# Kernel optimization log

Hardware: AMD Instinct MI355X
Metric: run time of the kernel (lower is better)

The kernel has to match this reference:

```python
import jax, jax.numpy as jnp
import numpy as np

M, K, N = 8192, 4096, 4096


def setup_inputs() -> dict:
    key = jax.random.key(0)
    k1, k2, k3 = jax.random.split(key, 3)
    x = jax.random.normal(k1, (M, K), dtype=jnp.float32)
    # int8 weight stored post-patch as [in_features, out_features] (cutlass [K, N] layout)
    weight = jax.random.randint(k2, (K, N), -128, 128, dtype=jnp.int32)
    bias = jax.random.normal(k3, (N,), dtype=jnp.float32) * 0.1
    # static per-tensor scales (scalar Parameters of shape [1])
    input_scale = jnp.array([0.02], dtype=jnp.float32)
    weight_scale = jnp.array([0.01], dtype=jnp.float32)
    return {"x": x, "weight": weight, "bias": bias,
            "input_scale": input_scale, "weight_scale": weight_scale}


def reference(x, weight, bias, input_scale, weight_scale):
    # ops.scaled_int8_quant(x, input_scale, symmetric=True):
    # static per-tensor symmetric quantization to int8
    x_q = jnp.clip(jnp.round(x / input_scale), -128, 127).astype(jnp.int8)  # [M, K]
    # scale_a * scale_b, fused bias add, output in x.dtype
    acc = jax.lax.dot_general(
        x_q, weight.astype(jnp.int8),
        dimension_numbers=(((1,), (0,)), ((), ())),
        preferred_element_type=jnp.int32,
    )  # [M, N] int32
    out = acc.astype(x.dtype) * (input_scale * weight_scale) + bias.astype(x.dtype)
    return out
```

## Files before the change

kernel.cpp:

```cpp
#include <hip/hip_runtime.h>
#include <hip/hip_bf16.h>


#define M_DIM 8192
#define K_DIM 4096
#define N_DIM 4096

typedef int i32x4 __attribute__((ext_vector_type(4)));

__device__ __forceinline__ void async_ld16(const void* g, void* l) {
  __builtin_amdgcn_global_load_lds(
      (const __attribute__((address_space(1))) void*)g,
      (__attribute__((address_space(3))) void*)l, 16, 0, 0);
}

__global__ __launch_bounds__(256) void quant_x(const float* __restrict__ x,
                                               const float* __restrict__ sptr,
                                               char* __restrict__ xq) {
  const float s = sptr[0];
  const size_t base = ((size_t)blockIdx.x * 256 + threadIdx.x) * 16;
  const float4* xv = (const float4*)(x + base);
  union { char c[16]; i32x4 v; } u;
#pragma unroll
  for (int q = 0; q < 4; ++q) {
    float4 f = xv[q];
    float a = fminf(127.f, fmaxf(-128.f, rintf(f.x / s)));
    float b = fminf(127.f, fmaxf(-128.f, rintf(f.y / s)));
    float c = fminf(127.f, fmaxf(-128.f, rintf(f.z / s)));
    float d = fminf(127.f, fmaxf(-128.f, rintf(f.w / s)));
    u.c[q * 4 + 0] = (char)(int)a;
    u.c[q * 4 + 1] = (char)(int)b;
    u.c[q * 4 + 2] = (char)(int)c;
    u.c[q * 4 + 3] = (char)(int)d;
  }
  *(i32x4*)(xq + base) = u.v;
}

__global__ __launch_bounds__(256) void wconv(const int* __restrict__ w,
                                             char* __restrict__ bt) {
  __shared__ alignas(16) char tile[64][80];
  const int k0 = blockIdx.x * 64;
  const int n0 = blockIdx.y * 64;
  const int t = threadIdx.x;
  const int kr = t >> 4;
  const int nc = (t & 15) * 4;
#pragma unroll
  for (int it = 0; it < 4; ++it) {
    int k = it * 16 + kr;
    int4 v = *(const int4*)(w + (size_t)(k0 + k) * N_DIM + n0 + nc);
    tile[nc + 0][k] = (char)v.x;
    tile[nc + 1][k] = (char)v.y;
    tile[nc + 2][k] = (char)v.z;
    tile[nc + 3][k] = (char)v.w;
  }
  __syncthreads();
  const int n = t >> 2;
  const int ks = (t & 3) * 16;
  int4 o = *(const int4*)&tile[n][ks];
  *(int4*)(bt + (size_t)(n0 + n) * K_DIM + k0 + ks) = o;
}

__global__ __launch_bounds__(256) void gemm_i8(
    const char* __restrict__ Aq, const char* __restrict__ Bt,
    const float* __restrict__ bias,
    const float* __restrict__ is_ptr, const float* __restrict__ ws_ptr,
    float* __restrict__ out) {
  __shared__ alignas(16) char ldsA[128 * 128];
  __shared__ alignas(16) char ldsB[128 * 128];

  const int nbn = N_DIM / 128;
  const int bid = blockIdx.x;
  const int cpx = gridDim.x >> 3;
  const int swz = (bid & 7) * cpx + (bid >> 3);
  const int bm0 = (swz / nbn) * 128;
  const int bn0 = (swz % nbn) * 128;

  const int t = threadIdx.x;
  const int lane = t & 63;
  const int wave = t >> 6;
  const int wm = wave >> 1;
  const int wn = wave & 1;
  const int lr = lane & 15;
  const int lkb = (lane >> 4) << 4;

  const int sr = t >> 3;
  const int sc = ((t & 7) ^ (sr & 7)) << 4;
  const char* aSrc = Aq + (size_t)(bm0 + sr) * K_DIM + sc;
  const char* bSrc = Bt + (size_t)(bn0 + sr) * K_DIM + sc;
  char* aDst = &ldsA[t * 16];
  char* bDst = &ldsB[t * 16];

  int aOff[4][2], bOff[4][2];
#pragma unroll
  for (int m = 0; m < 4; ++m) {
    int row = wm * 64 + m * 16 + lr;
#pragma unroll
    for (int ks = 0; ks < 2; ++ks) {
      int col = ks * 64 + lkb;
      aOff[m][ks] = row * 128 + (col ^ ((row & 7) << 4));
    }
  }
#pragma unroll
  for (int n = 0; n < 4; ++n) {
    int row = wn * 64 + n * 16 + lr;
#pragma unroll
    for (int ks = 0; ks < 2; ++ks) {
      int col = ks * 64 + lkb;
      bOff[n][ks] = row * 128 + (col ^ ((row & 7) << 4));
    }
  }

  i32x4 acc[4][4];
#pragma unroll
  for (int m = 0; m < 4; ++m)
#pragma unroll
    for (int n = 0; n < 4; ++n) acc[m][n] = (i32x4)(0);

  const int NT = K_DIM / 128;
  for (int kt = 0; kt < NT; ++kt) {
    const size_t ko = (size_t)kt * 128;
#pragma unroll
    for (int it = 0; it < 4; ++it) {
      async_ld16(aSrc + ko + (size_t)it * 32 * K_DIM, aDst + it * 4096);
      async_ld16(bSrc + ko + (size_t)it * 32 * K_DIM, bDst + it * 4096);
    }
    __syncthreads();
#pragma unroll
    for (int ks = 0; ks < 2; ++ks) {
      i32x4 aF[4], bF[4];
#pragma unroll
      for (int m = 0; m < 4; ++m) aF[m] = *(const i32x4*)&ldsA[aOff[m][ks]];
#pragma unroll
      for (int n = 0; n < 4; ++n) bF[n] = *(const i32x4*)&ldsB[bOff[n][ks]];
#pragma unroll
      for (int m = 0; m < 4; ++m)
#pragma unroll
        for (int n = 0; n < 4; ++n)
          acc[m][n] = __builtin_amdgcn_mfma_i32_16x16x64_i8(aF[m], bF[n],
                                                            acc[m][n], 0, 0, 0);
    }
    __syncthreads();
  }

  const float s = is_ptr[0] * ws_ptr[0];
  const int colBase = bn0 + wn * 64 + lr;
  float bv[4];
#pragma unroll
  for (int n = 0; n < 4; ++n) bv[n] = bias[colBase + n * 16];
  const int rowBase = bm0 + wm * 64 + ((lane >> 4) << 2);
#pragma unroll
  for (int m = 0; m < 4; ++m) {
#pragma unroll
    for (int j = 0; j < 4; ++j) {
      const int row = rowBase + m * 16 + j;
      float* orow = out + (size_t)row * N_DIM;
#pragma unroll
      for (int n = 0; n < 4; ++n)
        orow[colBase + n * 16] = (float)acc[m][n][j] * s + bv[n];
    }
  }
}

extern "C" void kernel_launch(void* const* d_in, const int* in_sizes, int n_in,
                              void* d_out, int out_size, void* d_ws, size_t ws_size,
                              hipStream_t stream) {
  const float* x    = (const float*)d_in[0];
  const int*   w    = (const int*)d_in[1];
  const float* bias = (const float*)d_in[2];
  const float* isc  = (const float*)d_in[3];
  const float* wsc  = (const float*)d_in[4];
  float* out = (float*)d_out;

  char* Aq = (char*)d_ws;
  char* Bt = (char*)d_ws + (size_t)M_DIM * K_DIM;

  quant_x<<<(M_DIM * K_DIM) / (256 * 16), 256, 0, stream>>>(x, isc, Aq);

  dim3 tg(K_DIM / 64, N_DIM / 64);
  wconv<<<tg, 256, 0, stream>>>(w, Bt);

  gemm_i8<<<(M_DIM / 128) * (N_DIM / 128), 256, 0, stream>>>(Aq, Bt, bias, isc,
                                                             wsc, out);
}
```

Before: 432.8 us.

## Rewrite int8 GEMM as 256x256 double-buffered 8-phase pipeline and repack weight conversion

```diff
diff --git a/kernel.cpp b/kernel.cpp
--- a/kernel.cpp
+++ b/kernel.cpp
@@ -36,139 +36,213 @@
   *(i32x4*)(xq + base) = u.v;
 }
 
-__global__ __launch_bounds__(256) void wconv(const int* __restrict__ w,
-                                             char* __restrict__ bt) {
-  __shared__ alignas(16) char tile[64][80];
-  const int k0 = blockIdx.x * 64;
+__global__ __launch_bounds__(256) void wconv2(const int* __restrict__ w,
+                                              char* __restrict__ bt) {
+  __shared__ unsigned int lt[16 * 132];
+  const int k0 = blockIdx.x * 128;
   const int n0 = blockIdx.y * 64;
   const int t = threadIdx.x;
+  const int n4 = t & 15;
   const int kr = t >> 4;
-  const int nc = (t & 15) * 4;
-#pragma unroll
-  for (int it = 0; it < 4; ++it) {
-    int k = it * 16 + kr;
-    int4 v = *(const int4*)(w + (size_t)(k0 + k) * N_DIM + n0 + nc);
-    tile[nc + 0][k] = (char)v.x;
-    tile[nc + 1][k] = (char)v.y;
-    tile[nc + 2][k] = (char)v.z;
-    tile[nc + 3][k] = (char)v.w;
+#pragma unroll
+  for (int i = 0; i < 8; ++i) {
+    int k = kr + i * 16;
+    int4 v = *(const int4*)(w + (size_t)(k0 + k) * N_DIM + n0 + n4 * 4);
+    unsigned int p = ((unsigned)v.x & 0xffu) | (((unsigned)v.y & 0xffu) << 8) |
+                     (((unsigned)v.z & 0xffu) << 16) | (((unsigned)v.w) << 24);
+    lt[n4 * 132 + k] = p;
   }
   __syncthreads();
   const int n = t >> 2;
-  const int ks = (t & 3) * 16;
-  int4 o = *(const int4*)&tile[n][ks];
-  *(int4*)(bt + (size_t)(n0 + n) * K_DIM + k0 + ks) = o;
-}
-
-__global__ __launch_bounds__(256) void gemm_i8(
+  const int n4r = n >> 2;
+  const unsigned int bsel = (unsigned)(n & 3);
+  const unsigned int sel01 = bsel * 0x101u + 0x0400u;
+#pragma unroll
+  for (int o = 0; o < 2; ++o) {
+    int ks = (t & 3) * 2 + o;
+    const unsigned int* base = &lt[n4r * 132 + ks * 16];
+    uint4 R;
+    unsigned int r[4];
+#pragma unroll
+    for (int g = 0; g < 4; ++g) {
+      uint4 W = *(const uint4*)(base + g * 4);
+      unsigned int t0 = __builtin_amdgcn_perm(W.y, W.x, sel01);
+      unsigned int t1 = __builtin_amdgcn_perm(W.w, W.z, sel01);
+      r[g] = __builtin_amdgcn_perm(t1, t0, 0x05040100u);
+    }
+    R.x = r[0]; R.y = r[1]; R.z = r[2]; R.w = r[3];
+    *(uint4*)(bt + (size_t)(n0 + n) * K_DIM + k0 + ks * 16) = R;
+  }
+}
+
+__global__ __launch_bounds__(512, 2) void gemm_i8_8ph(
     const char* __restrict__ Aq, const char* __restrict__ Bt,
-    const float* __restrict__ bias,
-    const float* __restrict__ is_ptr, const float* __restrict__ ws_ptr,
-    float* __restrict__ out) {
-  __shared__ alignas(16) char ldsA[128 * 128];
-  __shared__ alignas(16) char ldsB[128 * 128];
-
-  const int nbn = N_DIM / 128;
+    const float* __restrict__ bias, const float* __restrict__ is_ptr,
+    const float* __restrict__ ws_ptr, float* __restrict__ out) {
+  __shared__ alignas(16) char lds[131072];
+
+  const int nbn = N_DIM / 256;
   const int bid = blockIdx.x;
   const int cpx = gridDim.x >> 3;
   const int swz = (bid & 7) * cpx + (bid >> 3);
-  const int bm0 = (swz / nbn) * 128;
-  const int bn0 = (swz % nbn) * 128;
+  const int bm0 = (swz / nbn) * 256;
+  const int bn0 = (swz % nbn) * 256;
 
   const int t = threadIdx.x;
   const int lane = t & 63;
   const int wave = t >> 6;
-  const int wm = wave >> 1;
-  const int wn = wave & 1;
+  const int wm = wave >> 2;
+  const int wn = wave & 3;
   const int lr = lane & 15;
-  const int lkb = (lane >> 4) << 4;
-
-  const int sr = t >> 3;
-  const int sc = ((t & 7) ^ (sr & 7)) << 4;
-  const char* aSrc = Aq + (size_t)(bm0 + sr) * K_DIM + sc;
-  const char* bSrc = Bt + (size_t)(bn0 + sr) * K_DIM + sc;
-  char* aDst = &ldsA[t * 16];
-  char* bDst = &ldsB[t * 16];
-
-  int aOff[4][2], bOff[4][2];
-#pragma unroll
-  for (int m = 0; m < 4; ++m) {
-    int row = wm * 64 + m * 16 + lr;
-#pragma unroll
-    for (int ks = 0; ks < 2; ++ks) {
-      int col = ks * 64 + lkb;
-      aOff[m][ks] = row * 128 + (col ^ ((row & 7) << 4));
+  const int kg = lane >> 4;
+
+  const int r0 = t >> 3;
+  const int s0 = t & 7;
+  const int scol = ((s0 ^ (r0 & 7)) << 4);
+  const char* aStrip = Aq + (size_t)(bm0 + r0) * K_DIM + scol;
+  const char* bStrip = Bt + (size_t)(bn0 + r0) * K_DIM + scol;
+  const int dstBase = t * 16;
+
+  int sA[2];
+  sA[0] = ((kg ^ (lr & 7)) << 4);
+  sA[1] = (((4 + kg) ^ (lr & 7)) << 4);
+  const int aBase = (wm * 16 + lr) * 128;
+  const int bBase = 65536 + (wn * 16 + lr) * 128;
+
+#define STAGE(strip, matOff, dbuf, kt, half)                                  \
+  {                                                                           \
+    const char* s_ =                                                          \
+        (strip) + (size_t)(kt)*128 + (size_t)(half)*128 * K_DIM;              \
+    _Pragma("unroll") for (int j = 0; j < 2; ++j) async_ld16(                 \
+        s_ + (size_t)j * 64 * K_DIM,                                          \
+        &lds[(matOff) + (dbuf)*32768 + (half)*16384 + j * 8192 + dstBase]);   \
+  }
+
+#define LDA(mh, dbuf)                                                         \
+  _Pragma("unroll") for (int fi = 0; fi < 4; ++fi)                            \
+      _Pragma("unroll") for (int ks = 0; ks < 2; ++ks) aF[fi][ks] =           \
+      *(const i32x4*)&lds[(dbuf)*32768 + (mh)*16384 + fi * 4096 + aBase +     \
+                          sA[ks]];
+
+#define LDB(nh, dbuf)                                                         \
+  _Pragma("unroll") for (int gi = 0; gi < 2; ++gi)                            \
+      _Pragma("unroll") for (int ks = 0; ks < 2; ++ks) bF[gi][ks] =           \
+      *(const i32x4*)&lds[(dbuf)*32768 + (nh)*16384 + gi * 8192 + bBase +     \
+                          sA[ks]];
+
+#define MFMAQ(mh, nh)                                                         \
+  __builtin_amdgcn_s_setprio(1);                                              \
+  _Pragma("unroll") for (int ks = 0; ks < 2; ++ks)                            \
+      _Pragma("unroll") for (int fi = 0; fi < 4; ++fi)                        \
+          _Pragma("unroll") for (int gi = 0; gi < 2; ++gi) acc[(mh)*4 + fi]   \
+                                                              [(nh)*2 + gi] = \
+      __builtin_amdgcn_mfma_i32_16x16x64_i8(                                  \
+          aF[fi][ks], bF[gi][ks], acc[(mh)*4 + fi][(nh)*2 + gi], 0, 0, 0);    \
+  __builtin_amdgcn_s_setprio(0);
+
+#define FENCE asm volatile("" ::: "memory")
+#define BAR __builtin_amdgcn_s_barrier()
+#define WAITV(n) asm volatile("s_waitcnt vmcnt(" #n ")" ::: "memory")
+
+  i32x4 acc[8][4];
+#pragma unroll
+  for (int f = 0; f < 8; ++f)
+#pragma unroll
+    for (int g = 0; g < 4; ++g) acc[f][g] = (i32x4)(0);
+  i32x4 aF[4][2], bF[2][2];
+
+  STAGE(aStrip, 0, 0, 0, 0);
+  STAGE(aStrip, 0, 0, 0, 1);
+  STAGE(bStrip, 65536, 0, 0, 0);
+  STAGE(bStrip, 65536, 0, 0, 1);
+  STAGE(aStrip, 0, 1, 1, 0);
+  STAGE(bStrip, 65536, 1, 1, 1);
+  WAITV(4);
+  FENCE; BAR; FENCE;
+
+#pragma unroll 1
+  for (int i = 0; i < 15; ++i) {
+    const int T = 2 * i;
+    LDA(0, 0); LDB(0, 0);
+    STAGE(aStrip, 0, 1, T + 1, 1);
+    FENCE; BAR; MFMAQ(0, 0); FENCE; BAR;
+    LDB(1, 0);
+    STAGE(bStrip, 65536, 1, T + 1, 0);
+    FENCE; BAR; MFMAQ(0, 1); FENCE; BAR;
+    LDA(1, 0);
+    STAGE(aStrip, 0, 0, T + 2, 0);
+    FENCE; BAR; MFMAQ(1, 1); FENCE; BAR;
+    LDB(0, 0);
+    STAGE(bStrip, 65536, 0, T + 2, 1);
+    WAITV(4);
+    FENCE; BAR; MFMAQ(1, 0); FENCE; BAR;
+    LDA(0, 1); LDB(0, 1);
+    STAGE(aStrip, 0, 0, T + 2, 1);
+    FENCE; BAR; MFMAQ(0, 0); FENCE; BAR;
+    LDB(1, 1);
+    STAGE(bStrip, 65536, 0, T + 2, 0);
+    FENCE; BAR; MFMAQ(0, 1); FENCE; BAR;
+    LDA(1, 1);
+    STAGE(aStrip, 0, 1, T + 3, 0);
+    FENCE; BAR; MFMAQ(1, 1); FENCE; BAR;
+    LDB(0, 1);
+    STAGE(bStrip, 65536, 1, T + 3, 1);
+    WAITV(4);
+    FENCE; BAR; MFMAQ(1, 0); FENCE; BAR;
+  }
+
+  LDA(0, 0); LDB(0, 0);
+  STAGE(aStrip, 0, 1, 31, 1);
+  FENCE; BAR; MFMAQ(0, 0); FENCE; BAR;
+  LDB(1, 0);
+  STAGE(bStrip, 65536, 1, 31, 0);
+  FENCE; BAR; MFMAQ(0, 1); FENCE; BAR;
+  LDA(1, 0);
+  FENCE; BAR; MFMAQ(1, 1); FENCE; BAR;
+  LDB(0, 0);
+  WAITV(0);
+  FENCE; BAR; MFMAQ(1, 0); FENCE; BAR;
+  LDA(0, 1); LDB(0, 1);
+  FENCE; BAR; MFMAQ(0, 0); FENCE; BAR;
+  LDB(1, 1);
+  FENCE; BAR; MFMAQ(0, 1); FENCE; BAR;
+  LDA(1, 1);
+  FENCE; BAR; MFMAQ(1, 1); FENCE; BAR;
+  LDB(0, 1);
+  FENCE; BAR; MFMAQ(1, 0);
+
+  const float s = is_ptr[0] * ws_ptr[0];
+  float bv[4];
+#pragma unroll
+  for (int g = 0; g < 4; ++g) bv[g] = bias[bn0 + g * 64 + wn * 16 + lr];
+#pragma unroll
+  for (int f = 0; f < 8; ++f) {
+    const int crow0 = bm0 + f * 32 + wm * 16 + kg * 4;
+#pragma unroll
+    for (int j = 0; j < 4; ++j) {
+      float* orow = out + (size_t)(crow0 + j) * N_DIM;
+#pragma unroll
+      for (int g = 0; g < 4; ++g)
+        orow[bn0 + g * 64 + wn * 16 + lr] = (float)acc[f][g][j] * s + bv[g];
     }
   }
-#pragma unroll
-  for (int n = 0; n < 4; ++n) {
-    int row = wn * 64 + n * 16 + lr;
-#pragma unroll
-    for (int ks = 0; ks < 2; ++ks) {
-      int col = ks * 64 + lkb;
-      bOff[n][ks] = row * 128 + (col ^ ((row & 7) << 4));
-    }
-  }
-
-  i32x4 acc[4][4];
-#pragma unroll
-  for (int m = 0; m < 4; ++m)
-#pragma unroll
-    for (int n = 0; n < 4; ++n) acc[m][n] = (i32x4)(0);
-
-  const int NT = K_DIM / 128;
-  for (int kt = 0; kt < NT; ++kt) {
-    const size_t ko = (size_t)kt * 128;
-#pragma unroll
-    for (int it = 0; it < 4; ++it) {
-      async_ld16(aSrc + ko + (size_t)it * 32 * K_DIM, aDst + it * 4096);
-      async_ld16(bSrc + ko + (size_t)it * 32 * K_DIM, bDst + it * 4096);
-    }
-    __syncthreads();
-#pragma unroll
-    for (int ks = 0; ks < 2; ++ks) {
-      i32x4 aF[4], bF[4];
-#pragma unroll
-      for (int m = 0; m < 4; ++m) aF[m] = *(const i32x4*)&ldsA[aOff[m][ks]];
-#pragma unroll
-      for (int n = 0; n < 4; ++n) bF[n] = *(const i32x4*)&ldsB[bOff[n][ks]];
-#pragma unroll
-      for (int m = 0; m < 4; ++m)
-#pragma unroll
-        for (int n = 0; n < 4; ++n)
-          acc[m][n] = __builtin_amdgcn_mfma_i32_16x16x64_i8(aF[m], bF[n],
-                                                            acc[m][n], 0, 0, 0);
-    }
-    __syncthreads();
-  }
-
-  const float s = is_ptr[0] * ws_ptr[0];
-  const int colBase = bn0 + wn * 64 + lr;
-  float bv[4];
-#pragma unroll
-  for (int n = 0; n < 4; ++n) bv[n] = bias[colBase + n * 16];
-  const int rowBase = bm0 + wm * 64 + ((lane >> 4) << 2);
-#pragma unroll
-  for (int m = 0; m < 4; ++m) {
-#pragma unroll
-    for (int j = 0; j < 4; ++j) {
-      const int row = rowBase + m * 16 + j;
-      float* orow = out + (size_t)row * N_DIM;
-#pragma unroll
-      for (int n = 0; n < 4; ++n)
-        orow[colBase + n * 16] = (float)acc[m][n][j] * s + bv[n];
-    }
-  }
+#undef STAGE
+#undef LDA
+#undef LDB
+#undef MFMAQ
+#undef FENCE
+#undef BAR
+#undef WAITV
 }
 
 extern "C" void kernel_launch(void* const* d_in, const int* in_sizes, int n_in,
-                              void* d_out, int out_size, void* d_ws, size_t ws_size,
-                              hipStream_t stream) {
-  const float* x    = (const float*)d_in[0];
-  const int*   w    = (const int*)d_in[1];
+                              void* d_out, int out_size, void* d_ws,
+                              size_t ws_size, hipStream_t stream) {
+  const float* x = (const float*)d_in[0];
+  const int* w = (const int*)d_in[1];
   const float* bias = (const float*)d_in[2];
-  const float* isc  = (const float*)d_in[3];
-  const float* wsc  = (const float*)d_in[4];
+  const float* isc = (const float*)d_in[3];
+  const float* wsc = (const float*)d_in[4];
   float* out = (float*)d_out;
 
   char* Aq = (char*)d_ws;
@@ -176,9 +250,9 @@
 
   quant_x<<<(M_DIM * K_DIM) / (256 * 16), 256, 0, stream>>>(x, isc, Aq);
 
-  dim3 tg(K_DIM / 64, N_DIM / 64);
-  wconv<<<tg, 256, 0, stream>>>(w, Bt);
-
-  gemm_i8<<<(M_DIM / 128) * (N_DIM / 128), 256, 0, stream>>>(Aq, Bt, bias, isc,
-                                                             wsc, out);
-}
+  dim3 tg(K_DIM / 128, N_DIM / 64);
+  wconv2<<<tg, 256, 0, stream>>>(w, Bt);
+
+  gemm_i8_8ph<<<(M_DIM / 256) * (N_DIM / 256), 512, 0, stream>>>(
+      Aq, Bt, bias, isc, wsc, out);
+}
```

Result: faster. 396.1 us (-8.5%).
